# Kernel optimization log

Measured on AMD Instinct MI355X. Metric: run time of the kernel, lower is better.

## Reference

```python
import jax, jax.numpy as jnp
import numpy as np
from jax import lax

WINDOW_SIZE = 11
SIGMA = 1.5
MAX_VAL = 1.0


def _gaussian_kernel_2d(window_size: int, sigma: float) -> jnp.ndarray:
    coords = jnp.arange(window_size, dtype=jnp.float32) - window_size // 2
    g = jnp.exp(-coords ** 2 / (2.0 * sigma ** 2))
    g = g / g.sum()
    k2d = jnp.outer(g, g)
    return k2d / k2d.sum()  # [W, W]


def _depthwise_conv(x: jnp.ndarray, k2d: jnp.ndarray) -> jnp.ndarray:
    # x: [B, C, H, W]; depthwise (groups=C) conv with SAME padding
    C = x.shape[1]
    ws = k2d.shape[0]
    kernel = jnp.broadcast_to(k2d[None, None], (C, 1, ws, ws)).astype(x.dtype)  # [C,1,ws,ws]
    pad = ws // 2
    return lax.conv_general_dilated(
        x, kernel,
        window_strides=(1, 1),
        padding=((pad, pad), (pad, pad)),
        dimension_numbers=('NCHW', 'OIHW', 'NCHW'),
        feature_group_count=C,
    )


def setup_inputs() -> dict:
    key = jax.random.key(0)
    k1, k2 = jax.random.split(key)
    B, C, H, W = 16, 3, 512, 512
    sr = jax.random.uniform(k1, (B, C, H, W), dtype=jnp.float32)
    hr = jax.random.uniform(k2, (B, C, H, W), dtype=jnp.float32)
    return {"sr": sr, "hr": hr}


def reference(sr, hr):
    c1 = (0.01 * MAX_VAL) ** 2
    c2 = (0.03 * MAX_VAL) ** 2
    k2d = _gaussian_kernel_2d(WINDOW_SIZE, SIGMA)

    mu1 = _depthwise_conv(sr, k2d)
    mu2 = _depthwise_conv(hr, k2d)
    mu1_sq = mu1 ** 2
    mu2_sq = mu2 ** 2
    mu1_mu2 = mu1 * mu2
    sigma1_sq = _depthwise_conv(sr * sr, k2d) - mu1_sq
    sigma2_sq = _depthwise_conv(hr * hr, k2d) - mu2_sq
    sigma12 = _depthwise_conv(sr * hr, k2d) - mu1_mu2

    ssim_map = (2 * mu1_mu2 + c1) * (2 * sigma12 + c2) / (
        (mu1_sq + mu2_sq + c1) * (sigma1_sq + sigma2_sq + c2) + 1e-12)
    return 1.0 - ssim_map.mean()
```

## Files before the change

### kernel.cpp

```cpp
#include <hip/hip_runtime.h>


typedef __attribute__((ext_vector_type(2))) float  f32x2;
typedef __attribute__((ext_vector_type(4))) float  f32x4;
typedef __fp16 f16;
typedef __attribute__((ext_vector_type(2))) __fp16 h2v;
typedef __attribute__((ext_vector_type(4))) __fp16 h4;
typedef __attribute__((ext_vector_type(8))) __fp16 h8;

constexpr int IMG_H = 512;
constexpr int IMG_W = 512;
constexpr int PL    = IMG_H * IMG_W;
constexpr int NBC   = 48;
constexpr int TW    = 64;
constexpr int TH    = 32;
constexpr int NBLKX = IMG_W / TW;
constexpr int NBLKY = IMG_H / TH;
constexpr int NPERS = 1024;

constexpr int XP   = 104;
constexpr int XR   = 48;
constexpr int XQS  = XR * XP;
constexpr int HTP  = 72;
constexpr int HTQS = 64 * HTP;
constexpr int SMEMH = 4 * XQS;
static_assert(4 * HTQS <= SMEMH, "Ht must fit in X union");

constexpr float C1 = 1.0e-4f;
constexpr float C2 = 9.0e-4f;

#define BAR_LGKM() do {                                       \
    __builtin_amdgcn_sched_barrier(0);                        \
    asm volatile("s_waitcnt lgkmcnt(0)" ::: "memory");        \
    __builtin_amdgcn_s_barrier();                             \
    __builtin_amdgcn_sched_barrier(0);                        \
} while (0)

__device__ const float GW[11] = {
    0.00102838f, 0.00759876f, 0.03600077f, 0.10936070f, 0.21300553f,
    0.26601172f, 0.21300553f, 0.10936070f, 0.03600077f, 0.00759876f,
    0.00102838f};

__device__ __forceinline__ h8 ldfrag(const f16* __restrict__ gtab, int base) {
    h8 b;
#pragma unroll
    for (int i = 0; i < 8; ++i) b[i] = gtab[base + i];
    return b;
}

__device__ __forceinline__ void cvt_store(f16* __restrict__ smem, int o,
                                          const float4& a0f, const float4& a1f,
                                          const float4& b0f, const float4& b1f) {
    const f32x2* a0 = (const f32x2*)&a0f;
    const f32x2* a1 = (const f32x2*)&a1f;
    const f32x2* b0 = (const f32x2*)&b0f;
    const f32x2* b1 = (const f32x2*)&b1f;
    const f32x2 s0 = a0[0] * a0[0] + b0[0] * b0[0];
    const f32x2 s1 = a0[1] * a0[1] + b0[1] * b0[1];
    const f32x2 s2 = a1[0] * a1[0] + b1[0] * b1[0];
    const f32x2 s3 = a1[1] * a1[1] + b1[1] * b1[1];
    const f32x2 p0 = a0[0] * b0[0], p1 = a0[1] * b0[1];
    const f32x2 p2 = a1[0] * b1[0], p3 = a1[1] * b1[1];
    union { h2v h2[4]; h8 v; } uva, uvb, uss, uab;
    uva.h2[0] = __builtin_amdgcn_cvt_pkrtz(a0[0].x, a0[0].y);
    uva.h2[1] = __builtin_amdgcn_cvt_pkrtz(a0[1].x, a0[1].y);
    uva.h2[2] = __builtin_amdgcn_cvt_pkrtz(a1[0].x, a1[0].y);
    uva.h2[3] = __builtin_amdgcn_cvt_pkrtz(a1[1].x, a1[1].y);
    uvb.h2[0] = __builtin_amdgcn_cvt_pkrtz(b0[0].x, b0[0].y);
    uvb.h2[1] = __builtin_amdgcn_cvt_pkrtz(b0[1].x, b0[1].y);
    uvb.h2[2] = __builtin_amdgcn_cvt_pkrtz(b1[0].x, b1[0].y);
    uvb.h2[3] = __builtin_amdgcn_cvt_pkrtz(b1[1].x, b1[1].y);
    uss.h2[0] = __builtin_amdgcn_cvt_pkrtz(s0.x, s0.y);
    uss.h2[1] = __builtin_amdgcn_cvt_pkrtz(s1.x, s1.y);
    uss.h2[2] = __builtin_amdgcn_cvt_pkrtz(s2.x, s2.y);
    uss.h2[3] = __builtin_amdgcn_cvt_pkrtz(s3.x, s3.y);
    uab.h2[0] = __builtin_amdgcn_cvt_pkrtz(p0.x, p0.y);
    uab.h2[1] = __builtin_amdgcn_cvt_pkrtz(p1.x, p1.y);
    uab.h2[2] = __builtin_amdgcn_cvt_pkrtz(p2.x, p2.y);
    uab.h2[3] = __builtin_amdgcn_cvt_pkrtz(p3.x, p3.y);
    *(h8*)&smem[0 * XQS + o] = uva.v;
    *(h8*)&smem[1 * XQS + o] = uvb.v;
    *(h8*)&smem[2 * XQS + o] = uss.v;
    *(h8*)&smem[3 * XQS + o] = uab.v;
}

__global__ __launch_bounds__(64) void ssim_init(double* acc) {
    if (threadIdx.x == 0) acc[0] = 0.0;
}

__global__ __launch_bounds__(256, 4) void ssim_main(const float* __restrict__ sr,
                                                    const float* __restrict__ hr,
                                                    double* __restrict__ sink,
                                                    int mode) {
    __shared__ __align__(16) f16 smem[SMEMH];
    __shared__ __align__(8)  f16 gtab[128];
    __shared__ float wsums[4];

    const int tid  = threadIdx.x;
    const int w    = tid >> 6;
    const int lane = tid & 63;
    const int l15  = lane & 15;
    const int grp8 = (lane >> 4) << 3;
    const int grp4 = (lane >> 4) << 2;

    const int bx  = blockIdx.x & 7;
    const int by  = (blockIdx.x >> 3) & 15;
    const int bc0 = blockIdx.x >> 7;
    const int gr0 = by * TH - 5;
    const int gc0 = bx * TW - 8;

    const float* __restrict__ srp = sr + (size_t)bc0 * PL;
    const float* __restrict__ hrp = hr + (size_t)bc0 * PL;
    const size_t PSTEP = (size_t)8 * PL;

    const int tt0 = tid;
    const int tt1 = tid + 256;
    const bool t1v = (tid < 224);
    const int r_0 = tt0 / 10, c_0 = tt0 - 10 * r_0;
    const int r_1 = tt1 / 10, c_1 = tt1 - 10 * r_1;
    const int gr_0 = gr0 + r_0, gc_0 = gc0 + c_0 * 8;
    const int gr_1 = gr0 + r_1, gc_1 = gc0 + c_1 * 8;
    const bool ok0 = (r_0 < 42) & ((unsigned)gr_0 < (unsigned)IMG_H) &
                     ((unsigned)gc_0 < (unsigned)IMG_W);
    const bool ok1 = t1v & (r_1 < 42) & ((unsigned)gr_1 < (unsigned)IMG_H) &
                     ((unsigned)gc_1 < (unsigned)IMG_W);
    const int off0 = gr_0 * IMG_W + gc_0;
    const int off1 = gr_1 * IMG_W + gc_1;
    const int o0 = r_0 * XP + c_0 * 8;
    const int o1 = r_1 * XP + c_1 * 8;

    if (tid < 128) {
        const int d = tid - 66;
        float v = 0.f;
        if ((unsigned)d <= 10u) v = GW[d];
        gtab[tid] = (f16)v;
    }

    float s16 = 0.f;
#pragma unroll
    for (int d = 0; d <= 10; ++d) s16 += (float)(f16)GW[d];
    const float rs = 1.0f / (s16 * s16);

    float4 A0[2], A1[2], B0[2], B1[2];
#pragma unroll
    for (int t = 0; t < 2; ++t)
        A0[t] = A1[t] = B0[t] = B1[t] = (float4){0.f, 0.f, 0.f, 0.f};
    if (ok0) {
        const float4* pa = (const float4*)&srp[off0];
        const float4* pb = (const float4*)&hrp[off0];
        A0[0] = pa[0]; A1[0] = pa[1]; B0[0] = pb[0]; B1[0] = pb[1];
    }
    if (ok1) {
        const float4* pa = (const float4*)&srp[off1];
        const float4* pb = (const float4*)&hrp[off1];
        A0[1] = pa[0]; A1[1] = pa[1]; B0[1] = pb[0]; B1[1] = pb[1];
    }
    __syncthreads();

    const h8 bh = ldfrag(gtab, 63 + grp8 - l15);
    const h8 bv = ldfrag(gtab, 66 + grp8 - l15);

    float local = 0.f;

    for (int bc = bc0; bc < NBC; bc += 8) {
        cvt_store(smem, o0, A0[0], A1[0], B0[0], B1[0]);
        if (t1v) cvt_store(smem, o1, A0[1], A1[1], B0[1], B1[1]);

        BAR_LGKM();

        if (bc + 8 < NBC) {
            srp += PSTEP; hrp += PSTEP;
            if (ok0) {
                const float4* pa = (const float4*)&srp[off0];
                const float4* pb = (const float4*)&hrp[off0];
                A0[0] = pa[0]; A1[0] = pa[1]; B0[0] = pb[0]; B1[0] = pb[1];
            }
            if (ok1) {
                const float4* pa = (const float4*)&srp[off1];
                const float4* pb = (const float4*)&hrp[off1];
                A0[1] = pa[0]; A1[1] = pa[1]; B0[1] = pb[0]; B1[1] = pb[1];
            }
        }
        __builtin_amdgcn_sched_barrier(0);

        f32x4 acc[4][3] = {};
#pragma unroll
        for (int Mt = 0; Mt < 3; ++Mt) {
            const int arow = (16 * Mt + l15) * XP + 16 * w + grp8;
#pragma unroll
            for (int q = 0; q < 4; ++q) {
                const h8 af = *(const h8*)&smem[q * XQS + arow];
                acc[q][Mt] = __builtin_amdgcn_mfma_f32_16x16x32_f16(af, bh, acc[q][Mt], 0, 0, 0);
            }
        }

        BAR_LGKM();

#pragma unroll
        for (int q = 0; q < 4; ++q) {
#pragma unroll
            for (int Mt = 0; Mt < 3; ++Mt) {
                union { h2v h2[2]; h4 v; } u;
                u.h2[0] = __builtin_amdgcn_cvt_pkrtz(acc[q][Mt][0], acc[q][Mt][1]);
                u.h2[1] = __builtin_amdgcn_cvt_pkrtz(acc[q][Mt][2], acc[q][Mt][3]);
                *(h4*)&smem[q * HTQS + (16 * w + l15) * HTP + 16 * Mt + grp4] = u.v;
            }
        }

        f32x4 acc2[4][2] = {};
        const int abase = (16 * w + l15) * HTP + grp8;
#pragma unroll
        for (int q = 0; q < 4; ++q) {
            const h8 a0 = *(const h8*)&smem[q * HTQS + abase];
            const h8 a1 = *(const h8*)&smem[q * HTQS + abase + 16];
            acc2[q][0] = __builtin_amdgcn_mfma_f32_16x16x32_f16(a0, bv, acc2[q][0], 0, 0, 0);
            acc2[q][1] = __builtin_amdgcn_mfma_f32_16x16x32_f16(a1, bv, acc2[q][1], 0, 0, 0);
        }

#pragma unroll
        for (int nt = 0; nt < 2; ++nt) {
            const f32x4 m1 = acc2[0][nt] * rs;
            const f32x4 m2 = acc2[1][nt] * rs;
            const f32x4 S  = acc2[2][nt] * rs;
            const f32x4 pp = acc2[3][nt] * rs;
            const f32x4 mu1s = m1 * m1, mu2s = m2 * m2, mu12 = m1 * m2;
            const f32x4 sg12 = pp - mu12;
            const f32x4 sgs  = S - mu1s - mu2s;
            const f32x4 num = (2.f * mu12 + C1) * (2.f * sg12 + C2);
            const f32x4 den = (mu1s + mu2s + C1) * (sgs + C2) + 1e-12f;
#pragma unroll
            for (int e = 0; e < 4; ++e)
                local += num[e] * __builtin_amdgcn_rcpf(den[e]);
        }

        BAR_LGKM();
    }

#pragma unroll
    for (int offr = 32; offr > 0; offr >>= 1)
        local += __shfl_down(local, offr, 64);
    if ((tid & 63) == 0) wsums[tid >> 6] = local;
    __syncthreads();
    if (tid == 0) {
        const double bsum = (double)(wsums[0] + wsums[1] + wsums[2] + wsums[3]);
        if (mode == 0) {
            sink[blockIdx.x] = bsum;
        } else {
            atomicAdd(sink, bsum);
        }
    }
}

__global__ __launch_bounds__(256) void ssim_finalize(const double* __restrict__ partial,
                                                     float* __restrict__ out, int count) {
    __shared__ double ws[4];
    double s = 0.0;
    for (int i = threadIdx.x; i < count; i += 256) s += partial[i];
#pragma unroll
    for (int off = 32; off > 0; off >>= 1)
        s += __shfl_down(s, off, 64);
    const int lane = threadIdx.x & 63, wave = threadIdx.x >> 6;
    if (lane == 0) ws[wave] = s;
    __syncthreads();
    if (threadIdx.x == 0) {
        const double tot = ws[0] + ws[1] + ws[2] + ws[3];
        const double n = (double)NBC * IMG_H * IMG_W;
        out[0] = (float)(1.0 - tot / n);
    }
}

extern "C" void kernel_launch(void* const* d_in, const int* in_sizes, int n_in,
                              void* d_out, int out_size, void* d_ws, size_t ws_size,
                              hipStream_t stream) {
    const float* sr = (const float*)d_in[0];
    const float* hr = (const float*)d_in[1];
    float* out = (float*)d_out;

    if (ws_size >= (size_t)NPERS * sizeof(double)) {
        double* partial = (double*)d_ws;
        ssim_main<<<dim3(NPERS), dim3(256), 0, stream>>>(sr, hr, partial, 0);
        ssim_finalize<<<dim3(1), dim3(256), 0, stream>>>(partial, out, NPERS);
    } else {
        double* acc = (double*)d_ws;
        ssim_init<<<dim3(1), dim3(64), 0, stream>>>(acc);
        ssim_main<<<dim3(NPERS), dim3(256), 0, stream>>>(sr, hr, acc, 1);
        ssim_finalize<<<dim3(1), dim3(256), 0, stream>>>(acc, out, 1);
    }
}
```

Measured before the change: 126.3 us.

## Shrink tile height to 16 rows and raise occupancy to six blocks per CU

Tile height drops from 32 to 16 rows, which shrinks the shared-memory staging buffers and the accumulator arrays. The launch bound moves from 4 to 6 blocks per CU and the persistent grid grows from 1024 to 1536 blocks. The halo load is restructured: one row per thread, a few extra threads for the last row, and explicit zeroing of the MFMA padding rows. Smaller tiles raise the halo-to-output ratio, so more redundant input is read and more MFMA work is wasted per output pixel, traded against better latency hiding.

Result: slower. 132.3 us (+4.8%).

```diff
diff --git a/kernel.cpp b/kernel.cpp
--- a/kernel.cpp
+++ b/kernel.cpp
@@ -13,15 +13,14 @@
 constexpr int PL    = IMG_H * IMG_W;
 constexpr int NBC   = 48;
 constexpr int TW    = 64;
-constexpr int TH    = 32;
-constexpr int NBLKX = IMG_W / TW;
-constexpr int NBLKY = IMG_H / TH;
-constexpr int NPERS = 1024;
-
-constexpr int XP   = 104;
-constexpr int XR   = 48;
+constexpr int TH    = 16;
+constexpr int NPERS = 1536;
+constexpr int ITERS = (IMG_W / TW) * (IMG_H / TH) * NBC / NPERS;
+
+constexpr int XP   = 88;
+constexpr int XR   = 32;
 constexpr int XQS  = XR * XP;
-constexpr int HTP  = 72;
+constexpr int HTP  = 40;
 constexpr int HTQS = 64 * HTP;
 constexpr int SMEMH = 4 * XQS;
 static_assert(4 * HTQS <= SMEMH, "Ht must fit in X union");
@@ -88,7 +87,7 @@
     if (threadIdx.x == 0) acc[0] = 0.0;
 }
 
-__global__ __launch_bounds__(256, 4) void ssim_main(const float* __restrict__ sr,
+__global__ __launch_bounds__(256, 6) void ssim_main(const float* __restrict__ sr,
                                                     const float* __restrict__ hr,
                                                     double* __restrict__ sink,
                                                     int mode) {
@@ -104,30 +103,31 @@
     const int grp4 = (lane >> 4) << 2;
 
     const int bx  = blockIdx.x & 7;
-    const int by  = (blockIdx.x >> 3) & 15;
-    const int bc0 = blockIdx.x >> 7;
+    const int by  = (blockIdx.x >> 3) & 31;
+    const int bcg = blockIdx.x >> 8;
     const int gr0 = by * TH - 5;
     const int gc0 = bx * TW - 8;
 
-    const float* __restrict__ srp = sr + (size_t)bc0 * PL;
-    const float* __restrict__ hrp = hr + (size_t)bc0 * PL;
-    const size_t PSTEP = (size_t)8 * PL;
-
-    const int tt0 = tid;
-    const int tt1 = tid + 256;
-    const bool t1v = (tid < 224);
-    const int r_0 = tt0 / 10, c_0 = tt0 - 10 * r_0;
-    const int r_1 = tt1 / 10, c_1 = tt1 - 10 * r_1;
-    const int gr_0 = gr0 + r_0, gc_0 = gc0 + c_0 * 8;
-    const int gr_1 = gr0 + r_1, gc_1 = gc0 + c_1 * 8;
-    const bool ok0 = (r_0 < 42) & ((unsigned)gr_0 < (unsigned)IMG_H) &
+    const float* __restrict__ srp = sr + (size_t)bcg * PL;
+    const float* __restrict__ hrp = hr + (size_t)bcg * PL;
+    const size_t PSTEP = (size_t)6 * PL;
+
+    const int r0s = tid / 10, c0s = tid - 10 * r0s;
+    const int gr_0 = gr0 + r0s, gc_0 = gc0 + c0s * 8;
+    const bool ok0 = ((unsigned)gr_0 < (unsigned)IMG_H) &
                      ((unsigned)gc_0 < (unsigned)IMG_W);
-    const bool ok1 = t1v & (r_1 < 42) & ((unsigned)gr_1 < (unsigned)IMG_H) &
-                     ((unsigned)gc_1 < (unsigned)IMG_W);
     const int off0 = gr_0 * IMG_W + gc_0;
-    const int off1 = gr_1 * IMG_W + gc_1;
-    const int o0 = r_0 * XP + c_0 * 8;
-    const int o1 = r_1 * XP + c_1 * 8;
+    const int o0   = r0s * XP + c0s * 8;
+
+    const int cx   = 6 + tid;
+    const int grx  = gr0 + 25, gcx = gc0 + cx * 8;
+    const bool okx = (tid < 4) & ((unsigned)grx < (unsigned)IMG_H) &
+                     ((unsigned)gcx < (unsigned)IMG_W);
+    const int offx = grx * IMG_W + gcx;
+    const int ox   = 25 * XP + cx * 8;
+
+    const int rz = 26 + tid / 10, cz = tid - 10 * (tid / 10);
+    const int oz = rz * XP + cz * 8;
 
     if (tid < 128) {
         const int d = tid - 66;
@@ -141,19 +141,12 @@
     for (int d = 0; d <= 10; ++d) s16 += (float)(f16)GW[d];
     const float rs = 1.0f / (s16 * s16);
 
-    float4 A0[2], A1[2], B0[2], B1[2];
-#pragma unroll
-    for (int t = 0; t < 2; ++t)
-        A0[t] = A1[t] = B0[t] = B1[t] = (float4){0.f, 0.f, 0.f, 0.f};
+    float4 La0, La1, Lb0, Lb1;
+    La0 = La1 = Lb0 = Lb1 = (float4){0.f, 0.f, 0.f, 0.f};
     if (ok0) {
         const float4* pa = (const float4*)&srp[off0];
         const float4* pb = (const float4*)&hrp[off0];
-        A0[0] = pa[0]; A1[0] = pa[1]; B0[0] = pb[0]; B1[0] = pb[1];
-    }
-    if (ok1) {
-        const float4* pa = (const float4*)&srp[off1];
-        const float4* pb = (const float4*)&hrp[off1];
-        A0[1] = pa[0]; A1[1] = pa[1]; B0[1] = pb[0]; B1[1] = pb[1];
+        La0 = pa[0]; La1 = pa[1]; Lb0 = pb[0]; Lb1 = pb[1];
     }
     __syncthreads();
 
@@ -162,30 +155,41 @@
 
     float local = 0.f;
 
-    for (int bc = bc0; bc < NBC; bc += 8) {
-        cvt_store(smem, o0, A0[0], A1[0], B0[0], B1[0]);
-        if (t1v) cvt_store(smem, o1, A0[1], A1[1], B0[1], B1[1]);
+    for (int it = 0; it < ITERS; ++it) {
+        if (tid < 4) {
+            float4 ea0, ea1, eb0, eb1;
+            ea0 = ea1 = eb0 = eb1 = (float4){0.f, 0.f, 0.f, 0.f};
+            if (okx) {
+                const float4* pa = (const float4*)&srp[offx];
+                const float4* pb = (const float4*)&hrp[offx];
+                ea0 = pa[0]; ea1 = pa[1]; eb0 = pb[0]; eb1 = pb[1];
+            }
+            cvt_store(smem, ox, ea0, ea1, eb0, eb1);
+        }
+        cvt_store(smem, o0, La0, La1, Lb0, Lb1);
+        if (tid < 60) {
+            const h8 z = {};
+            *(h8*)&smem[0 * XQS + oz] = z;
+            *(h8*)&smem[1 * XQS + oz] = z;
+            *(h8*)&smem[2 * XQS + oz] = z;
+            *(h8*)&smem[3 * XQS + oz] = z;
+        }
 
         BAR_LGKM();
 
-        if (bc + 8 < NBC) {
+        if (it < ITERS - 1) {
             srp += PSTEP; hrp += PSTEP;
             if (ok0) {
                 const float4* pa = (const float4*)&srp[off0];
                 const float4* pb = (const float4*)&hrp[off0];
-                A0[0] = pa[0]; A1[0] = pa[1]; B0[0] = pb[0]; B1[0] = pb[1];
-            }
-            if (ok1) {
-                const float4* pa = (const float4*)&srp[off1];
-                const float4* pb = (const float4*)&hrp[off1];
-                A0[1] = pa[0]; A1[1] = pa[1]; B0[1] = pb[0]; B1[1] = pb[1];
+                La0 = pa[0]; La1 = pa[1]; Lb0 = pb[0]; Lb1 = pb[1];
             }
         }
         __builtin_amdgcn_sched_barrier(0);
 
-        f32x4 acc[4][3] = {};
-#pragma unroll
-        for (int Mt = 0; Mt < 3; ++Mt) {
+        f32x4 acc[4][2] = {};
+#pragma unroll
+        for (int Mt = 0; Mt < 2; ++Mt) {
             const int arow = (16 * Mt + l15) * XP + 16 * w + grp8;
 #pragma unroll
             for (int q = 0; q < 4; ++q) {
@@ -199,7 +203,7 @@
 #pragma unroll
         for (int q = 0; q < 4; ++q) {
 #pragma unroll
-            for (int Mt = 0; Mt < 3; ++Mt) {
+            for (int Mt = 0; Mt < 2; ++Mt) {
                 union { h2v h2[2]; h4 v; } u;
                 u.h2[0] = __builtin_amdgcn_cvt_pkrtz(acc[q][Mt][0], acc[q][Mt][1]);
                 u.h2[1] = __builtin_amdgcn_cvt_pkrtz(acc[q][Mt][2], acc[q][Mt][3]);
@@ -207,22 +211,19 @@
             }
         }
 
-        f32x4 acc2[4][2] = {};
+        f32x4 acc2[4] = {};
         const int abase = (16 * w + l15) * HTP + grp8;
 #pragma unroll
         for (int q = 0; q < 4; ++q) {
             const h8 a0 = *(const h8*)&smem[q * HTQS + abase];
-            const h8 a1 = *(const h8*)&smem[q * HTQS + abase + 16];
-            acc2[q][0] = __builtin_amdgcn_mfma_f32_16x16x32_f16(a0, bv, acc2[q][0], 0, 0, 0);
-            acc2[q][1] = __builtin_amdgcn_mfma_f32_16x16x32_f16(a1, bv, acc2[q][1], 0, 0, 0);
-        }
-
-#pragma unroll
-        for (int nt = 0; nt < 2; ++nt) {
-            const f32x4 m1 = acc2[0][nt] * rs;
-            const f32x4 m2 = acc2[1][nt] * rs;
-            const f32x4 S  = acc2[2][nt] * rs;
-            const f32x4 pp = acc2[3][nt] * rs;
+            acc2[q] = __builtin_amdgcn_mfma_f32_16x16x32_f16(a0, bv, acc2[q], 0, 0, 0);
+        }
+
+        {
+            const f32x4 m1 = acc2[0] * rs;
+            const f32x4 m2 = acc2[1] * rs;
+            const f32x4 S  = acc2[2] * rs;
+            const f32x4 pp = acc2[3] * rs;
             const f32x4 mu1s = m1 * m1, mu2s = m2 * m2, mu12 = m1 * m2;
             const f32x4 sg12 = pp - mu12;
             const f32x4 sgs  = S - mu1s - mu2s;
```
